# Kernel tuning notes

Measured on AMD Instinct MI355X. Metric: run time of the kernel, lower is better.

The kernel has to match this reference:

```python
import jax, jax.numpy as jnp
import numpy as np

TOP_K_FRACTION = 0.1


def setup_inputs() -> dict:
    key = jax.random.key(0)
    k1, k2, k3 = jax.random.split(key, 3)
    B, H, S, D = 2, 12, 1024, 64
    q = jax.random.normal(k1, (B, H, S, D), dtype=jnp.float32)
    k = jax.random.normal(k2, (B, H, S, D), dtype=jnp.float32)
    v = jax.random.normal(k3, (B, H, S, D), dtype=jnp.float32)
    mask = jnp.zeros((B, 1, 1, S), dtype=jnp.float32)
    return {"q": q, "k": k, "v": v, "mask": mask}


def reference(q, k, v, mask):
    B, H, S, D = q.shape
    k_precise = max(1, int(S * TOP_K_FRACTION))
    # binary (sign) approximation of attention scores; detached like torch
    q_bin = jnp.sign(jax.lax.stop_gradient(q))
    k_bin = jnp.sign(jax.lax.stop_gradient(k))
    approx_scores = jnp.einsum('bhsd,bhtd->bhst', q_bin, k_bin) / D  # [B,H,S,S]
    _, topk_idx = jax.lax.top_k(approx_scores, k_precise)  # [B,H,S,kp]
    # gather top-k keys/values per query: [B,H,S,kp,D]
    k_gathered = jnp.take_along_axis(k[:, :, None, :, :], topk_idx[..., None], axis=3)
    v_gathered = jnp.take_along_axis(v[:, :, None, :, :], topk_idx[..., None], axis=3)
    scale = np.float32(1.0 / np.sqrt(D))
    precise_scores = jnp.einsum('bhsd,bhskd->bhsk', q, k_gathered) * scale
    # gather mask along key positions: mask [B,1,1,S] -> [B,H,S,kp]
    mask_gathered = jnp.take_along_axis(
        jnp.broadcast_to(mask, (B, H, S, S)), topk_idx, axis=-1)
    precise_scores = precise_scores + mask_gathered
    precise_probs = jax.nn.softmax(precise_scores, axis=-1)
    attn_output = jnp.einsum('bhsk,bhskd->bhsd', precise_probs, v_gathered)
    return attn_output
```

## Files before the change

### kernel.cpp

```cpp
#include <hip/hip_runtime.h>
#include <hip/hip_fp16.h>
#include <cstdint>

#define BB 2
#define HH 12
#define SS 1024
#define DD 64
#define KP 102
#define QT 64
#define CHK 128
#define NCHUNK 8
#define KROW 72
#define VROW 136

typedef _Float16 half8v  __attribute__((ext_vector_type(8)));
typedef float    float4v __attribute__((ext_vector_type(4)));
typedef unsigned long long u64;

__device__ __forceinline__ int mbcnt64(u64 m) {
    return (int)__builtin_amdgcn_mbcnt_hi((unsigned)(m >> 32),
               __builtin_amdgcn_mbcnt_lo((unsigned)(m & 0xffffffffull), 0u));
}
template <int CTRL>
__device__ __forceinline__ float dpp_f(float x) {
    return __builtin_bit_cast(float,
        __builtin_amdgcn_update_dpp(0, __builtin_bit_cast(int, x), CTRL, 0xF, 0xF, false));
}
__device__ __forceinline__ float row16_sum(float x) {
    x += dpp_f<0xB1>(x);
    x += dpp_f<0x4E>(x);
    x += dpp_f<0x141>(x);
    x += dpp_f<0x140>(x);
    return x;
}

__global__ __launch_bounds__(256) void pack_kernel(
    const float* __restrict__ k, const float* __restrict__ v,
    u64* __restrict__ kbits, _Float16* __restrict__ kh, _Float16* __restrict__ vT)
{
    int row  = (int)((blockIdx.x * 256 + threadIdx.x) >> 6);
    int lane = (int)(threadIdx.x & 63);
    if (row >= BB * HH * SS) return;
    float kv = k[(size_t)row * DD + lane];
    float vv = v[(size_t)row * DD + lane];
    u64 km = __ballot(kv > 0.0f);
    kh[(size_t)row * DD + lane] = (_Float16)kv;
    int bh = row >> 10, t = row & (SS - 1);
    vT[((size_t)bh * DD + lane) * SS + t] = (_Float16)vv;
    if (lane == 0) kbits[row] = km;
}

__global__ __launch_bounds__(256, 2) void battn_kernel(
    const float* __restrict__ q, const _Float16* __restrict__ kh,
    const _Float16* __restrict__ vT, const float* __restrict__ mask,
    const u64* __restrict__ kbits, float* __restrict__ out)
{
    const int tid  = (int)threadIdx.x;
    const int w    = tid >> 6;
    const int lane = tid & 63;
    const int bh    = (int)blockIdx.x >> 4;
    const int qtile = (int)blockIdx.x & 15;
    const int bidx  = bh / HH;
    const int qr    = lane & 15;
    const int quad  = lane >> 4;

    __shared__ __align__(16) _Float16 K_lds[CHK * KROW];
    __shared__ __align__(16) _Float16 VT_lds[DD * VROW];
    __shared__ __align__(16) _Float16 P_lds[4][16 * VROW];
    __shared__ u64  selmask[QT][16];
    __shared__ __align__(16) float mask_lds[SS];

    {
        const float* mrow = mask + (size_t)bidx * SS;
        float4v mv = *(const float4v*)(mrow + tid * 4);
        mv[0] -= 4.0f; mv[1] -= 4.0f; mv[2] -= 4.0f; mv[3] -= 4.0f;
        *(float4v*)(&mask_lds[tid * 4]) = mv;
    }

    const u64* kb = kbits + (size_t)bh * SS;
    u64 kbreg[16];
    #pragma unroll
    for (int j = 0; j < 16; ++j) kbreg[j] = kb[j * 64 + lane];
    const float* qwave = q + ((size_t)bh * SS + qtile * QT + w * 16) * DD;

    #pragma unroll 1
    for (int qq = 0; qq < 16; ++qq) {
        float qv = qwave[qq * DD + lane];
        u64 qm = __ballot(qv > 0.0f);
        int pbin[16];
        #pragma unroll
        for (int j = 0; j < 16; ++j) pbin[j] = (int)__popcll(qm ^ kbreg[j]);
        #define COUNT_LE(P, OUTC)                                      \
            { int _c = 0;                                              \
              _Pragma("unroll")                                        \
              for (int j = 0; j < 16; ++j)                             \
                  _c += (int)__popcll(__ballot(pbin[j] <= (P)));       \
              (OUTC) = _c; }
        int P = 27, c, clt;
        COUNT_LE(P, c);
        if (c >= KP) {
            COUNT_LE(P - 1, clt);
            while (clt >= KP) { c = clt; --P; COUNT_LE(P - 1, clt); }
        } else {
            do { clt = c; ++P; COUNT_LE(P, c); } while (c < KP);
        }
        const int binP = P;
        const int need = KP - clt;
        #undef COUNT_LE
        u64 my_tm = 0; int tie_base = 0;
        #pragma unroll
        for (int j = 0; j < 16; ++j) {
            bool isGt  = pbin[j] < binP;
            bool isTie = (pbin[j] == binP);
            u64 tiem = __ballot(isTie);
            int rank = tie_base + mbcnt64(tiem);
            bool take = isGt || (isTie && rank < need);
            u64 tm = __ballot(take);
            if (lane == j) my_tm = tm;
            tie_base += (int)__popcll(tiem);
        }
        if (lane < 16) selmask[w * 16 + qq][lane] = my_tm;
    }

    half8v qa0, qa1;
    {
        const float* qf = qwave + qr * DD + quad * 8;
        #pragma unroll
        for (int j = 0; j < 8; ++j) {
            qa0[j] = (_Float16)(qf[j] * 0.125f);
            qa1[j] = (_Float16)(qf[32 + j] * 0.125f);
        }
    }

    const _Float16* khead  = kh + (size_t)bh * SS * DD;
    const _Float16* vthead = vT + (size_t)bh * DD * SS;

    float4v acc[4];
    #pragma unroll
    for (int dt = 0; dt < 4; ++dt) { acc[dt][0]=0.f; acc[dt][1]=0.f; acc[dt][2]=0.f; acc[dt][3]=0.f; }
    float lp[4] = {0.f, 0.f, 0.f, 0.f};

    #pragma unroll 1
    for (int ch = 0; ch < NCHUNK; ++ch) {
        __syncthreads();
        #pragma unroll
        for (int it = 0; it < 4; ++it) {
            int s = tid + it * 256;
            int row = s >> 3, c8 = s & 7;
            *(half8v*)(&K_lds[row * KROW + c8 * 8]) =
                *(const half8v*)(khead + (size_t)(ch * CHK + row) * DD + c8 * 8);
        }
        #pragma unroll
        for (int it = 0; it < 4; ++it) {
            int s = tid + it * 256;
            int d = s >> 4, c8 = s & 15;
            *(half8v*)(&VT_lds[d * VROW + c8 * 8]) =
                *(const half8v*)(vthead + (size_t)d * SS + ch * CHK + c8 * 8);
        }
        __syncthreads();

        #pragma unroll
        for (int nt = 0; nt < 8; ++nt) {
            const _Float16* kl = &K_lds[(nt * 16 + qr) * KROW + quad * 8];
            half8v b0 = *(const half8v*)kl;
            half8v b1 = *(const half8v*)(kl + 32);
            float4v cfr; cfr[0]=0.f; cfr[1]=0.f; cfr[2]=0.f; cfr[3]=0.f;
            cfr = __builtin_amdgcn_mfma_f32_16x16x32_f16(qa0, b0, cfr, 0, 0, 0);
            cfr = __builtin_amdgcn_mfma_f32_16x16x32_f16(qa1, b1, cfr, 0, 0, 0);
            const int tg   = ch * CHK + nt * 16 + qr;
            const float mk = mask_lds[tg];
            const int w32  = tg >> 5, b32 = tg & 31;
            #pragma unroll
            for (int r = 0; r < 4; ++r) {
                unsigned sm = ((const unsigned*)selmask[w * 16 + quad * 4 + r])[w32];
                float e = ((sm >> b32) & 1u) ? __expf(cfr[r] + mk) : 0.0f;
                lp[r] += e;
                P_lds[w][(quad * 4 + r) * VROW + nt * 16 + qr] = (_Float16)e;
            }
        }

        half8v pa0 = *(const half8v*)(&P_lds[w][qr * VROW +  0 + quad * 8]);
        half8v pa1 = *(const half8v*)(&P_lds[w][qr * VROW + 32 + quad * 8]);
        half8v pa2 = *(const half8v*)(&P_lds[w][qr * VROW + 64 + quad * 8]);
        half8v pa3 = *(const half8v*)(&P_lds[w][qr * VROW + 96 + quad * 8]);
        #pragma unroll
        for (int dt = 0; dt < 4; ++dt) {
            const _Float16* vl = &VT_lds[(dt * 16 + qr) * VROW + quad * 8];
            acc[dt] = __builtin_amdgcn_mfma_f32_16x16x32_f16(pa0, *(const half8v*)(vl +  0), acc[dt], 0, 0, 0);
            acc[dt] = __builtin_amdgcn_mfma_f32_16x16x32_f16(pa1, *(const half8v*)(vl + 32), acc[dt], 0, 0, 0);
            acc[dt] = __builtin_amdgcn_mfma_f32_16x16x32_f16(pa2, *(const half8v*)(vl + 64), acc[dt], 0, 0, 0);
            acc[dt] = __builtin_amdgcn_mfma_f32_16x16x32_f16(pa3, *(const half8v*)(vl + 96), acc[dt], 0, 0, 0);
        }
    }

    float rinv[4];
    #pragma unroll
    for (int r = 0; r < 4; ++r) rinv[r] = __frcp_rn(row16_sum(lp[r]));

    float* orow = out + ((size_t)bh * SS + qtile * QT + w * 16) * DD;
    #pragma unroll
    for (int dt = 0; dt < 4; ++dt)
        #pragma unroll
        for (int r = 0; r < 4; ++r)
            orow[(quad * 4 + r) * DD + dt * 16 + qr] = acc[dt][r] * rinv[r];
}

extern "C" void kernel_launch(void* const* d_in, const int* in_sizes, int n_in,
                              void* d_out, int out_size, void* d_ws, size_t ws_size,
                              hipStream_t stream) {
    const float* q    = (const float*)d_in[0];
    const float* k    = (const float*)d_in[1];
    const float* v    = (const float*)d_in[2];
    const float* mask = (const float*)d_in[3];
    float* out = (float*)d_out;

    const int rows = BB * HH * SS;
    u64* kbits = (u64*)d_ws;
    _Float16* kh = (_Float16*)((char*)d_ws + (size_t)rows * sizeof(u64));
    _Float16* vT = kh + (size_t)rows * DD;

    pack_kernel<<<(rows * 64 + 255) / 256, 256, 0, stream>>>(k, v, kbits, kh, vT);
    battn_kernel<<<BB * HH * (SS / QT), 256, 0, stream>>>(q, kh, vT, mask, kbits, out);
}
```

Measured before the change: 131.1 us.

## Split key range across two wave halves and transpose V through LDS in pack

```diff
diff --git a/kernel.cpp b/kernel.cpp
--- a/kernel.cpp
+++ b/kernel.cpp
@@ -7,11 +7,9 @@
 #define SS 1024
 #define DD 64
 #define KP 102
-#define QT 64
-#define CHK 128
-#define NCHUNK 8
+#define CHK 64
 #define KROW 72
-#define VROW 136
+#define COMBW 65
 
 typedef _Float16 half8v  __attribute__((ext_vector_type(8)));
 typedef float    float4v __attribute__((ext_vector_type(4)));
@@ -38,19 +36,36 @@
     const float* __restrict__ k, const float* __restrict__ v,
     u64* __restrict__ kbits, _Float16* __restrict__ kh, _Float16* __restrict__ vT)
 {
-    int row  = (int)((blockIdx.x * 256 + threadIdx.x) >> 6);
-    int lane = (int)(threadIdx.x & 63);
-    if (row >= BB * HH * SS) return;
-    float kv = k[(size_t)row * DD + lane];
-    float vv = v[(size_t)row * DD + lane];
-    u64 km = __ballot(kv > 0.0f);
-    kh[(size_t)row * DD + lane] = (_Float16)kv;
-    int bh = row >> 10, t = row & (SS - 1);
-    vT[((size_t)bh * DD + lane) * SS + t] = (_Float16)vv;
-    if (lane == 0) kbits[row] = km;
-}
-
-__global__ __launch_bounds__(256, 2) void battn_kernel(
+    __shared__ __align__(16) _Float16 vt_lds[DD * KROW];
+    const int tid  = (int)threadIdx.x;
+    const int w    = tid >> 6;
+    const int lane = tid & 63;
+    const int bh = (int)blockIdx.x >> 4;
+    const int t0 = ((int)blockIdx.x & 15) * 64;
+
+    const float* kbase = k + ((size_t)bh * SS + t0) * DD;
+    const float* vbase = v + ((size_t)bh * SS + t0) * DD;
+    #pragma unroll 1
+    for (int i = 0; i < 16; ++i) {
+        int rl = w * 16 + i;
+        float kv = kbase[rl * DD + lane];
+        float vv = vbase[rl * DD + lane];
+        u64 km = __ballot(kv > 0.0f);
+        kh[((size_t)bh * SS + t0 + rl) * DD + lane] = (_Float16)kv;
+        vt_lds[lane * KROW + rl] = (_Float16)vv;
+        if (lane == 0) kbits[(size_t)bh * SS + t0 + rl] = km;
+    }
+    __syncthreads();
+    #pragma unroll
+    for (int it = 0; it < 2; ++it) {
+        int s = tid + it * 256;
+        int d = s >> 3, c8 = s & 7;
+        *(half8v*)(vT + ((size_t)bh * DD + d) * SS + t0 + c8 * 8) =
+            *(const half8v*)(&vt_lds[d * KROW + c8 * 8]);
+    }
+}
+
+__global__ __launch_bounds__(512, 4) void battn_kernel(
     const float* __restrict__ q, const _Float16* __restrict__ kh,
     const _Float16* __restrict__ vT, const float* __restrict__ mask,
     const u64* __restrict__ kbits, float* __restrict__ out)
@@ -63,68 +78,76 @@
     const int bidx  = bh / HH;
     const int qr    = lane & 15;
     const int quad  = lane >> 4;
-
-    __shared__ __align__(16) _Float16 K_lds[CHK * KROW];
-    __shared__ __align__(16) _Float16 VT_lds[DD * VROW];
-    __shared__ __align__(16) _Float16 P_lds[4][16 * VROW];
-    __shared__ u64  selmask[QT][16];
-    __shared__ __align__(16) float mask_lds[SS];
+    const int half  = w >> 2;
+    const int wq    = w & 3;
+
+    __shared__ __align__(16) char smem[65536];
+    _Float16* K0  = (_Float16*)(smem);
+    _Float16* VT0 = (_Float16*)(smem + 9216);
+    _Float16* K1  = (_Float16*)(smem + 18432);
+    _Float16* VT1 = (_Float16*)(smem + 27648);
+    _Float16* Pw  = (_Float16*)(smem + 36864) + w * 16 * KROW;
+    u64*      sel = (u64*)(smem + 55296);
+    _Float16* mlds = (_Float16*)(smem + 63488);
+    float* combA = (float*)(smem);
+    float* combL = (float*)(smem + 64 * COMBW * 4);
 
     {
-        const float* mrow = mask + (size_t)bidx * SS;
-        float4v mv = *(const float4v*)(mrow + tid * 4);
-        mv[0] -= 4.0f; mv[1] -= 4.0f; mv[2] -= 4.0f; mv[3] -= 4.0f;
-        *(float4v*)(&mask_lds[tid * 4]) = mv;
-    }
-
-    const u64* kb = kbits + (size_t)bh * SS;
-    u64 kbreg[16];
-    #pragma unroll
-    for (int j = 0; j < 16; ++j) kbreg[j] = kb[j * 64 + lane];
-    const float* qwave = q + ((size_t)bh * SS + qtile * QT + w * 16) * DD;
-
-    #pragma unroll 1
-    for (int qq = 0; qq < 16; ++qq) {
-        float qv = qwave[qq * DD + lane];
-        u64 qm = __ballot(qv > 0.0f);
-        int pbin[16];
-        #pragma unroll
-        for (int j = 0; j < 16; ++j) pbin[j] = (int)__popcll(qm ^ kbreg[j]);
-        #define COUNT_LE(P, OUTC)                                      \
-            { int _c = 0;                                              \
-              _Pragma("unroll")                                        \
-              for (int j = 0; j < 16; ++j)                             \
-                  _c += (int)__popcll(__ballot(pbin[j] <= (P)));       \
-              (OUTC) = _c; }
-        int P = 27, c, clt;
-        COUNT_LE(P, c);
-        if (c >= KP) {
-            COUNT_LE(P - 1, clt);
-            while (clt >= KP) { c = clt; --P; COUNT_LE(P - 1, clt); }
-        } else {
-            do { clt = c; ++P; COUNT_LE(P, c); } while (c < KP);
-        }
-        const int binP = P;
-        const int need = KP - clt;
-        #undef COUNT_LE
-        u64 my_tm = 0; int tie_base = 0;
-        #pragma unroll
-        for (int j = 0; j < 16; ++j) {
-            bool isGt  = pbin[j] < binP;
-            bool isTie = (pbin[j] == binP);
-            u64 tiem = __ballot(isTie);
-            int rank = tie_base + mbcnt64(tiem);
-            bool take = isGt || (isTie && rank < need);
-            u64 tm = __ballot(take);
-            if (lane == j) my_tm = tm;
-            tie_base += (int)__popcll(tiem);
-        }
-        if (lane < 16) selmask[w * 16 + qq][lane] = my_tm;
+        float2 mv = *(const float2*)(mask + (size_t)bidx * SS + tid * 2);
+        mlds[tid * 2]     = (_Float16)(mv.x - 4.0f);
+        mlds[tid * 2 + 1] = (_Float16)(mv.y - 4.0f);
+    }
+
+    const float* qblock = q + ((size_t)bh * SS + qtile * 64) * DD;
+    {
+        const u64* kb = kbits + (size_t)bh * SS;
+        u64 kbreg[16];
+        #pragma unroll
+        for (int j = 0; j < 16; ++j) kbreg[j] = kb[j * 64 + lane];
+        #pragma unroll 1
+        for (int qq = 0; qq < 8; ++qq) {
+            const int ql = w * 8 + qq;
+            float qv = qblock[ql * DD + lane];
+            u64 qm = __ballot(qv > 0.0f);
+            int pbin[16];
+            #pragma unroll
+            for (int j = 0; j < 16; ++j) pbin[j] = (int)__popcll(qm ^ kbreg[j]);
+            #define COUNT_LE(P, OUTC)                                      \
+                { int _c = 0;                                              \
+                  _Pragma("unroll")                                        \
+                  for (int j = 0; j < 16; ++j)                             \
+                      _c += (int)__popcll(__ballot(pbin[j] <= (P)));       \
+                  (OUTC) = _c; }
+            int P = 27, c, clt;
+            COUNT_LE(P, c);
+            if (c >= KP) {
+                COUNT_LE(P - 1, clt);
+                while (clt >= KP) { c = clt; --P; COUNT_LE(P - 1, clt); }
+            } else {
+                do { clt = c; ++P; COUNT_LE(P, c); } while (c < KP);
+            }
+            const int binP = P;
+            const int need = KP - clt;
+            #undef COUNT_LE
+            u64 my_tm = 0; int tie_base = 0;
+            #pragma unroll
+            for (int j = 0; j < 16; ++j) {
+                bool isGt  = pbin[j] < binP;
+                bool isTie = (pbin[j] == binP);
+                u64 tiem = __ballot(isTie);
+                int rank = tie_base + mbcnt64(tiem);
+                bool take = isGt || (isTie && rank < need);
+                u64 tm = __ballot(take);
+                if (lane == j) my_tm = tm;
+                tie_base += (int)__popcll(tiem);
+            }
+            if (lane < 16) sel[ql * 16 + lane] = my_tm;
+        }
     }
 
     half8v qa0, qa1;
     {
-        const float* qf = qwave + qr * DD + quad * 8;
+        const float* qf = qblock + (wq * 16 + qr) * DD + quad * 8;
         #pragma unroll
         for (int j = 0; j < 8; ++j) {
             qa0[j] = (_Float16)(qf[j] * 0.125f);
@@ -134,6 +157,7 @@
 
     const _Float16* khead  = kh + (size_t)bh * SS * DD;
     const _Float16* vthead = vT + (size_t)bh * DD * SS;
+    const int srow = tid >> 3, sc8 = tid & 7;
 
     float4v acc[4];
     #pragma unroll
@@ -141,68 +165,80 @@
     float lp[4] = {0.f, 0.f, 0.f, 0.f};
 
     #pragma unroll 1
-    for (int ch = 0; ch < NCHUNK; ++ch) {
+    for (int it = 0; it < 8; ++it) {
         __syncthreads();
-        #pragma unroll
-        for (int it = 0; it < 4; ++it) {
-            int s = tid + it * 256;
-            int row = s >> 3, c8 = s & 7;
-            *(half8v*)(&K_lds[row * KROW + c8 * 8]) =
-                *(const half8v*)(khead + (size_t)(ch * CHK + row) * DD + c8 * 8);
-        }
-        #pragma unroll
-        for (int it = 0; it < 4; ++it) {
-            int s = tid + it * 256;
-            int d = s >> 4, c8 = s & 15;
-            *(half8v*)(&VT_lds[d * VROW + c8 * 8]) =
-                *(const half8v*)(vthead + (size_t)d * SS + ch * CHK + c8 * 8);
-        }
+        *(half8v*)(K0  + srow * KROW + sc8 * 8) =
+            *(const half8v*)(khead + (size_t)(it * CHK + srow) * DD + sc8 * 8);
+        *(half8v*)(K1  + srow * KROW + sc8 * 8) =
+            *(const half8v*)(khead + (size_t)((it + 8) * CHK + srow) * DD + sc8 * 8);
+        *(half8v*)(VT0 + srow * KROW + sc8 * 8) =
+            *(const half8v*)(vthead + (size_t)srow * SS + it * CHK + sc8 * 8);
+        *(half8v*)(VT1 + srow * KROW + sc8 * 8) =
+            *(const half8v*)(vthead + (size_t)srow * SS + (it + 8) * CHK + sc8 * 8);
         __syncthreads();
 
-        #pragma unroll
-        for (int nt = 0; nt < 8; ++nt) {
-            const _Float16* kl = &K_lds[(nt * 16 + qr) * KROW + quad * 8];
-            half8v b0 = *(const half8v*)kl;
-            half8v b1 = *(const half8v*)(kl + 32);
+        const _Float16* KL = half ? K1 : K0;
+        const _Float16* VL = half ? VT1 : VT0;
+        const int ch = half * 8 + it;
+
+        #pragma unroll
+        for (int nt = 0; nt < 4; ++nt) {
+            const _Float16* klp = KL + (nt * 16 + qr) * KROW + quad * 8;
+            half8v b0 = *(const half8v*)klp;
+            half8v b1 = *(const half8v*)(klp + 32);
             float4v cfr; cfr[0]=0.f; cfr[1]=0.f; cfr[2]=0.f; cfr[3]=0.f;
             cfr = __builtin_amdgcn_mfma_f32_16x16x32_f16(qa0, b0, cfr, 0, 0, 0);
             cfr = __builtin_amdgcn_mfma_f32_16x16x32_f16(qa1, b1, cfr, 0, 0, 0);
-            const int tg   = ch * CHK + nt * 16 + qr;
-            const float mk = mask_lds[tg];
-            const int w32  = tg >> 5, b32 = tg & 31;
+            const int tg = ch * CHK + nt * 16 + qr;
+            const float mk = (float)mlds[tg];
             #pragma unroll
             for (int r = 0; r < 4; ++r) {
-                unsigned sm = ((const unsigned*)selmask[w * 16 + quad * 4 + r])[w32];
-                float e = ((sm >> b32) & 1u) ? __expf(cfr[r] + mk) : 0.0f;
+                const int qlr = wq * 16 + quad * 4 + r;
+                unsigned sm = ((const unsigned*)sel)[qlr * 32 + (tg >> 5)];
+                float e = ((sm >> (tg & 31)) & 1u) ? __expf(cfr[r] + mk) : 0.0f;
                 lp[r] += e;
-                P_lds[w][(quad * 4 + r) * VROW + nt * 16 + qr] = (_Float16)e;
+                Pw[(quad * 4 + r) * KROW + nt * 16 + qr] = (_Float16)e;
             }
         }
 
-        half8v pa0 = *(const half8v*)(&P_lds[w][qr * VROW +  0 + quad * 8]);
-        half8v pa1 = *(const half8v*)(&P_lds[w][qr * VROW + 32 + quad * 8]);
-        half8v pa2 = *(const half8v*)(&P_lds[w][qr * VROW + 64 + quad * 8]);
-        half8v pa3 = *(const half8v*)(&P_lds[w][qr * VROW + 96 + quad * 8]);
+        half8v pa0 = *(const half8v*)(Pw + qr * KROW + quad * 8);
+        half8v pa1 = *(const half8v*)(Pw + qr * KROW + 32 + quad * 8);
         #pragma unroll
         for (int dt = 0; dt < 4; ++dt) {
-            const _Float16* vl = &VT_lds[(dt * 16 + qr) * VROW + quad * 8];
-            acc[dt] = __builtin_amdgcn_mfma_f32_16x16x32_f16(pa0, *(const half8v*)(vl +  0), acc[dt], 0, 0, 0);
+            const _Float16* vl = VL + (dt * 16 + qr) * KROW + quad * 8;
+            acc[dt] = __builtin_amdgcn_mfma_f32_16x16x32_f16(pa0, *(const half8v*)vl,        acc[dt], 0, 0, 0);
             acc[dt] = __builtin_amdgcn_mfma_f32_16x16x32_f16(pa1, *(const half8v*)(vl + 32), acc[dt], 0, 0, 0);
-            acc[dt] = __builtin_amdgcn_mfma_f32_16x16x32_f16(pa2, *(const half8v*)(vl + 64), acc[dt], 0, 0, 0);
-            acc[dt] = __builtin_amdgcn_mfma_f32_16x16x32_f16(pa3, *(const half8v*)(vl + 96), acc[dt], 0, 0, 0);
-        }
-    }
-
-    float rinv[4];
+        }
+    }
+
+    __syncthreads();
     #pragma unroll
-    for (int r = 0; r < 4; ++r) rinv[r] = __frcp_rn(row16_sum(lp[r]));
-
-    float* orow = out + ((size_t)bh * SS + qtile * QT + w * 16) * DD;
-    #pragma unroll
-    for (int dt = 0; dt < 4; ++dt)
+    for (int r = 0; r < 4; ++r) lp[r] = row16_sum(lp[r]);
+    if (half == 0) {
+        if (qr == 0) {
+            #pragma unroll
+            for (int r = 0; r < 4; ++r) combL[wq * 16 + quad * 4 + r] = lp[r];
+        }
+        #pragma unroll
+        for (int dt = 0; dt < 4; ++dt)
+            #pragma unroll
+            for (int r = 0; r < 4; ++r)
+                combA[(wq * 16 + quad * 4 + r) * COMBW + dt * 16 + qr] = acc[dt][r];
+    }
+    __syncthreads();
+    if (half == 1) {
+        float rinv[4];
         #pragma unroll
         for (int r = 0; r < 4; ++r)
-            orow[(quad * 4 + r) * DD + dt * 16 + qr] = acc[dt][r] * rinv[r];
+            rinv[r] = __frcp_rn(lp[r] + combL[wq * 16 + quad * 4 + r]);
+        float* orow = out + ((size_t)bh * SS + qtile * 64 + wq * 16) * DD;
+        #pragma unroll
+        for (int dt = 0; dt < 4; ++dt)
+            #pragma unroll
+            for (int r = 0; r < 4; ++r)
+                orow[(quad * 4 + r) * DD + dt * 16 + qr] =
+                    (acc[dt][r] + combA[(wq * 16 + quad * 4 + r) * COMBW + dt * 16 + qr]) * rinv[r];
+    }
 }
 
 extern "C" void kernel_launch(void* const* d_in, const int* in_sizes, int n_in,
@@ -219,6 +255,6 @@
     _Float16* kh = (_Float16*)((char*)d_ws + (size_t)rows * sizeof(u64));
     _Float16* vT = kh + (size_t)rows * DD;
 
-    pack_kernel<<<(rows * 64 + 255) / 256, 256, 0, stream>>>(k, v, kbits, kh, vT);
-    battn_kernel<<<BB * HH * (SS / QT), 256, 0, stream>>>(q, kh, vT, mask, kbits, out);
-}
+    pack_kernel<<<rows / 64, 256, 0, stream>>>(k, v, kbits, kh, vT);
+    battn_kernel<<<BB * HH * (SS / 64), 512, 0, stream>>>(q, kh, vT, mask, kbits, out);
+}
```

New measurement: 117.0 us. 10.8% less time.
